# Kernel optimization log

Measured on AMD Instinct MI355X. Metric: run time of the kernel, lower is better.

The kernel has to match this reference:

```python
import jax, jax.numpy as jnp
from jax import lax
import numpy as np

B, IN, OUT = 32768, 512, 512


def _bit_length(a):
    # a: nonnegative int32. Smear high bit down, then popcount == bit length.
    y = a
    y = y | (y >> 1)
    y = y | (y >> 2)
    y = y | (y >> 4)
    y = y | (y >> 8)
    y = y | (y >> 16)
    return lax.population_count(y)


def trunc_top_bits(v, k=4):
    # compress_top4(|a|,|b|,4): keep top-k significant bits of each magnitude.
    a = jnp.abs(v)
    shift = jnp.maximum(_bit_length(a) - k, 0)
    t = (a >> shift) << shift
    return t * jnp.sign(v)


def setup_inputs() -> dict:
    key = jax.random.key(0)
    k1, k2, k3 = jax.random.split(key, 3)
    bound = 1.0 / np.sqrt(IN)  # matches kaiming_uniform(a=sqrt(5)) + bias bound
    x = jax.random.normal(k1, (B, IN), dtype=jnp.float32)
    weight = jax.random.uniform(k2, (OUT, IN), dtype=jnp.float32, minval=-bound, maxval=bound)
    bias = jax.random.uniform(k3, (OUT,), dtype=jnp.float32, minval=-bound, maxval=bound)
    return {"x": x, "weight": weight, "bias": bias, "weight_sf": 8, "act_sf": 6}


def reference(x, weight, bias, weight_sf, act_sf):
    # Fixed-point quantization: input / 2^{-sf} then trunc-toward-zero int cast
    xi = (x * (2.0 ** act_sf)).astype(jnp.int32)       # [B, IN]
    wi = (weight * (2.0 ** weight_sf)).astype(jnp.int32)  # [OUT, IN]
    # sign/abs decomposition + top-4-bit truncated multiply-accumulate:
    # sum_y compress_top4(|xi|,|wi|) * sign(xi)*sign(wi) == dot of signed truncs
    tx = trunc_top_bits(xi).astype(jnp.float32)
    tw = trunc_top_bits(wi).astype(jnp.float32)
    acc = jnp.einsum("bi,oi->bo", tx, tw)             # [B, OUT], exact in fp32
    scale = (2.0 ** (-act_sf)) * (2.0 ** (-weight_sf))
    return acc * scale + bias[None, :]
```

## Files before the change

kernel.cpp:

```cpp
#include <hip/hip_runtime.h>
#include <hip/hip_bf16.h>
#include <stdint.h>

#define B_DIM 32768
#define IN_DIM 512
#define OUT_DIM 512

typedef __bf16 bf16;
typedef bf16 bf16x8 __attribute__((ext_vector_type(8)));
typedef float f32x4 __attribute__((ext_vector_type(4)));

__device__ __forceinline__ uint32_t quant2(float a, float b, float scale) {
    uint32_t ua = __float_as_uint(truncf(a * scale)) & 0xFFF00000u;
    uint32_t ub = __float_as_uint(truncf(b * scale)) & 0xFFF00000u;
    return (ua >> 16) | (ub & 0xFFFF0000u);
}

__global__ void quant_kernel(const float* __restrict__ in, bf16* __restrict__ out,
                             int n4, const int* __restrict__ sf) {
    int i = blockIdx.x * blockDim.x + threadIdx.x;
    if (i >= n4) return;
    float scale = (float)(1 << *sf);
    float4 v = ((const float4*)in)[i];
    uint2 p;
    p.x = quant2(v.x, v.y, scale);
    p.y = quant2(v.z, v.w, scale);
    ((uint2*)out)[i] = p;
}

__global__ __launch_bounds__(256, 4)
void gemm_fused(const float* __restrict__ X, const bf16* __restrict__ QW,
                const float* __restrict__ bias, float* __restrict__ C,
                const int* __restrict__ wsf, const int* __restrict__ asf) {
    __shared__ bf16 As[128 * 64];
    __shared__ bf16 Bs[128 * 64];

    const int t    = threadIdx.x;
    const int w    = t >> 6;
    const int lane = t & 63;

    const int b    = blockIdx.x;
    const int xcd  = b & 7;
    const int slot = b >> 3;
    const int bm   = xcd * 32 + (slot >> 2);
    const int bn   = slot & 3;
    const int row0 = bm * 128;
    const int col0 = bn * 128;
    const int wm   = (w & 1) * 64;
    const int wn   = (w >> 1) * 64;

    const int ldr = t >> 3;
    const int ldc = (t & 7) * 8;

    const float* Xbase = X  + (size_t)row0 * IN_DIM;
    const bf16*  Wbase = QW + (size_t)col0 * IN_DIM;

    const float ascale = (float)(1 << *asf);

    f32x4 acc[4][4];
    for (int mt = 0; mt < 4; ++mt)
        for (int nt = 0; nt < 4; ++nt)
            acc[mt][nt] = 0.0f;

    for (int k0 = 0; k0 < IN_DIM; k0 += 64) {
        #pragma unroll
        for (int i = 0; i < 4; ++i) {
            const bf16* gb = Wbase + (size_t)(i * 32 + ldr) * IN_DIM + k0 + ldc;
            bf16*       lb = Bs + i * 2048 + w * 512;
            __builtin_amdgcn_global_load_lds((const __attribute__((address_space(1))) void*)gb,
                                             (__attribute__((address_space(3))) void*)lb, 16, 0, 0);
        }
        #pragma unroll
        for (int i = 0; i < 4; ++i) {
            const float* g = Xbase + (size_t)(i * 32 + ldr) * IN_DIM + k0 + ldc;
            float4 v0 = ((const float4*)g)[0];
            float4 v1 = ((const float4*)g)[1];
            uint4 p;
            p.x = quant2(v0.x, v0.y, ascale);
            p.y = quant2(v0.z, v0.w, ascale);
            p.z = quant2(v1.x, v1.y, ascale);
            p.w = quant2(v1.z, v1.w, ascale);
            *(uint4*)(As + (i * 32 + ldr) * 64 + ldc) = p;
        }
        __syncthreads();

        #pragma unroll
        for (int ks = 0; ks < 2; ++ks) {
            const int kcol = ks * 32 + (lane >> 4) * 8;
            const int arow = wm + (lane & 15);
            const int brow = wn + (lane & 15);
            bf16x8 af[4], bf[4];
            #pragma unroll
            for (int mt = 0; mt < 4; ++mt)
                af[mt] = *(const bf16x8*)(As + (arow + mt * 16) * 64 + kcol);
            #pragma unroll
            for (int nt = 0; nt < 4; ++nt)
                bf[nt] = *(const bf16x8*)(Bs + (brow + nt * 16) * 64 + kcol);
            #pragma unroll
            for (int mt = 0; mt < 4; ++mt)
                #pragma unroll
                for (int nt = 0; nt < 4; ++nt)
                    acc[mt][nt] = __builtin_amdgcn_mfma_f32_16x16x32_bf16(af[mt], bf[nt], acc[mt][nt], 0, 0, 0);
        }
        __syncthreads();
    }

    const float oscale = ldexpf(1.0f, -(*wsf + *asf));
    const int cl = lane & 15;
    const int rg = (lane >> 4) * 4;
    #pragma unroll
    for (int nt = 0; nt < 4; ++nt) {
        const int col = col0 + wn + nt * 16 + cl;
        const float bv = bias[col];
        #pragma unroll
        for (int mt = 0; mt < 4; ++mt) {
            f32x4 a = acc[mt][nt];
            #pragma unroll
            for (int r = 0; r < 4; ++r) {
                const int row = row0 + wm + mt * 16 + rg + r;
                C[(size_t)row * OUT_DIM + col] = a[r] * oscale + bv;
            }
        }
    }
}

extern "C" void kernel_launch(void* const* d_in, const int* in_sizes, int n_in,
                              void* d_out, int out_size, void* d_ws, size_t ws_size,
                              hipStream_t stream) {
    const float* x    = (const float*)d_in[0];
    const float* wgt  = (const float*)d_in[1];
    const float* bias = (const float*)d_in[2];
    const int*   wsf  = (const int*)d_in[3];
    const int*   asf  = (const int*)d_in[4];

    bf16* tw = (bf16*)d_ws;

    const int nw4 = OUT_DIM * IN_DIM / 4;
    quant_kernel<<<(nw4 + 255) / 256, 256, 0, stream>>>(wgt, tw, nw4, wsf);

    const int grid = (B_DIM / 128) * (OUT_DIM / 128);
    gemm_fused<<<grid, 256, 0, stream>>>(x, tw, bias, (float*)d_out, wsf, asf);
}
```

Measured before the change: 157.7 us.

## Pre-quantize activations in a separate pass and load both operands directly to LDS

Activation quantization moves out of the GEMM main loop into its own elementwise kernel that writes bf16 to the workspace. The GEMM then streams both A and W through global_load_lds into LDS with an XOR-swizzled layout meant to avoid bank conflicts. The quantization itself now packs the two values with a single byte-permute plus a mask. In exchange, the activations take an extra round trip through global memory: 64 MB of fp32 read plus 32 MB of bf16 written and read back. The old approach instead redundantly re-read and re-quantized X for each of the four column blocks.

```diff
diff --git a/kernel.cpp b/kernel.cpp
--- a/kernel.cpp
+++ b/kernel.cpp
@@ -11,9 +11,10 @@
 typedef float f32x4 __attribute__((ext_vector_type(4)));
 
 __device__ __forceinline__ uint32_t quant2(float a, float b, float scale) {
-    uint32_t ua = __float_as_uint(truncf(a * scale)) & 0xFFF00000u;
-    uint32_t ub = __float_as_uint(truncf(b * scale)) & 0xFFF00000u;
-    return (ua >> 16) | (ub & 0xFFFF0000u);
+    uint32_t ua = __float_as_uint(truncf(a * scale));
+    uint32_t ub = __float_as_uint(truncf(b * scale));
+    uint32_t p = __builtin_amdgcn_perm(ub, ua, 0x07060302u);
+    return p & 0xFFF0FFF0u;
 }
 
 __global__ void quant_kernel(const float* __restrict__ in, bf16* __restrict__ out,
@@ -29,9 +30,9 @@
 }
 
 __global__ __launch_bounds__(256, 4)
-void gemm_fused(const float* __restrict__ X, const bf16* __restrict__ QW,
-                const float* __restrict__ bias, float* __restrict__ C,
-                const int* __restrict__ wsf, const int* __restrict__ asf) {
+void gemm_bt(const bf16* __restrict__ A, const bf16* __restrict__ W,
+             const float* __restrict__ bias, float* __restrict__ C,
+             const int* __restrict__ wsf, const int* __restrict__ asf) {
     __shared__ bf16 As[128 * 64];
     __shared__ bf16 Bs[128 * 64];
 
@@ -49,58 +50,51 @@
     const int wm   = (w & 1) * 64;
     const int wn   = (w >> 1) * 64;
 
-    const int ldr = t >> 3;
-    const int ldc = (t & 7) * 8;
-
-    const float* Xbase = X  + (size_t)row0 * IN_DIM;
-    const bf16*  Wbase = QW + (size_t)col0 * IN_DIM;
-
-    const float ascale = (float)(1 << *asf);
+    const int m_st = t >> 3;
+    const int ku   = (t & 7) ^ (m_st & 7);
+    const size_t offA = (size_t)(row0 + m_st) * IN_DIM + ku * 8;
+    const size_t offB = (size_t)(col0 + m_st) * IN_DIM + ku * 8;
 
     f32x4 acc[4][4];
+    #pragma unroll
     for (int mt = 0; mt < 4; ++mt)
+        #pragma unroll
         for (int nt = 0; nt < 4; ++nt)
             acc[mt][nt] = 0.0f;
 
     for (int k0 = 0; k0 < IN_DIM; k0 += 64) {
         #pragma unroll
         for (int i = 0; i < 4; ++i) {
-            const bf16* gb = Wbase + (size_t)(i * 32 + ldr) * IN_DIM + k0 + ldc;
-            bf16*       lb = Bs + i * 2048 + w * 512;
+            const bf16* ga = A + offA + (size_t)i * 32 * IN_DIM + k0;
+            bf16*       la = As + (i * 256 + w * 64) * 8;
+            __builtin_amdgcn_global_load_lds((const __attribute__((address_space(1))) void*)ga,
+                                             (__attribute__((address_space(3))) void*)la, 16, 0, 0);
+            const bf16* gb = W + offB + (size_t)i * 32 * IN_DIM + k0;
+            bf16*       lb = Bs + (i * 256 + w * 64) * 8;
             __builtin_amdgcn_global_load_lds((const __attribute__((address_space(1))) void*)gb,
                                              (__attribute__((address_space(3))) void*)lb, 16, 0, 0);
         }
-        #pragma unroll
-        for (int i = 0; i < 4; ++i) {
-            const float* g = Xbase + (size_t)(i * 32 + ldr) * IN_DIM + k0 + ldc;
-            float4 v0 = ((const float4*)g)[0];
-            float4 v1 = ((const float4*)g)[1];
-            uint4 p;
-            p.x = quant2(v0.x, v0.y, ascale);
-            p.y = quant2(v0.z, v0.w, ascale);
-            p.z = quant2(v1.x, v1.y, ascale);
-            p.w = quant2(v1.z, v1.w, ascale);
-            *(uint4*)(As + (i * 32 + ldr) * 64 + ldc) = p;
-        }
         __syncthreads();
 
+        const int q  = lane >> 4;
+        const int rl = lane & 15;
+        const int sx = rl & 7;
         #pragma unroll
         for (int ks = 0; ks < 2; ++ks) {
-            const int kcol = ks * 32 + (lane >> 4) * 8;
-            const int arow = wm + (lane & 15);
-            const int brow = wn + (lane & 15);
-            bf16x8 af[4], bf[4];
+            const int c = ks * 4 + q;
+            const int cs = (c ^ sx) * 8;
+            bf16x8 af[4], bfr[4];
             #pragma unroll
             for (int mt = 0; mt < 4; ++mt)
-                af[mt] = *(const bf16x8*)(As + (arow + mt * 16) * 64 + kcol);
+                af[mt] = *(const bf16x8*)(As + (wm + mt * 16 + rl) * 64 + cs);
             #pragma unroll
             for (int nt = 0; nt < 4; ++nt)
-                bf[nt] = *(const bf16x8*)(Bs + (brow + nt * 16) * 64 + kcol);
+                bfr[nt] = *(const bf16x8*)(Bs + (wn + nt * 16 + rl) * 64 + cs);
             #pragma unroll
             for (int mt = 0; mt < 4; ++mt)
                 #pragma unroll
                 for (int nt = 0; nt < 4; ++nt)
-                    acc[mt][nt] = __builtin_amdgcn_mfma_f32_16x16x32_bf16(af[mt], bf[nt], acc[mt][nt], 0, 0, 0);
+                    acc[mt][nt] = __builtin_amdgcn_mfma_f32_16x16x32_bf16(af[mt], bfr[nt], acc[mt][nt], 0, 0, 0);
         }
         __syncthreads();
     }
@@ -133,11 +127,14 @@
     const int*   wsf  = (const int*)d_in[3];
     const int*   asf  = (const int*)d_in[4];
 
-    bf16* tw = (bf16*)d_ws;
+    bf16* tx = (bf16*)d_ws;
+    bf16* tw = (bf16*)((char*)d_ws + (size_t)B_DIM * IN_DIM * sizeof(bf16));
 
+    const int nx4 = B_DIM * IN_DIM / 4;
     const int nw4 = OUT_DIM * IN_DIM / 4;
+    quant_kernel<<<(nx4 + 255) / 256, 256, 0, stream>>>(x, tx, nx4, asf);
     quant_kernel<<<(nw4 + 255) / 256, 256, 0, stream>>>(wgt, tw, nw4, wsf);
 
     const int grid = (B_DIM / 128) * (OUT_DIM / 128);
-    gemm_fused<<<grid, 256, 0, stream>>>(x, tw, bias, (float*)d_out, wsf, asf);
+    gemm_bt<<<grid, 256, 0, stream>>>(tx, tw, bias, (float*)d_out, wsf, asf);
 }
```

Result: faster. 137.9 us (-12.6%).
